# Kernel tuning notes

Measured on AMD Instinct MI355X. Metric: run time of the kernel, lower is better.

Reference implementation:

```python
import jax, jax.numpy as jnp
import numpy as np
from jax import lax

EPS = 1e-10

def _ln(x, g, b):
    m = x.mean(-1, keepdims=True)
    v = x.var(-1, keepdims=True)
    return (x - m) / jnp.sqrt(v + 1e-5) * g + b

def _gather(t, idx):
    # t: (B, HW, c), idx: (B, HW, d) -> (B, HW, d, c); out[n,i,k,:] = t[n, idx[n,i,k], :]
    return jax.vmap(lambda tn, In: tn[In])(t, idx)

def setup_inputs() -> dict:
    key = jax.random.key(0)
    ks = jax.random.split(key, 20)
    b, v, c, d, h, w, hid, ksz = 2, 2, 128, 64, 64, 64, 256, 5
    hw = h * w
    Bf = b * v  # v_1 == 1 target view per reference view
    std = 0.02
    return {
        'features_mv': jax.random.normal(ks[0], (b, v, c, h, w), jnp.float32),
        'warp_indices': jax.random.randint(ks[1], (Bf, hw, d), 0, hw, jnp.int32),
        'depth_prob': jax.random.uniform(ks[2], (Bf, hw, d), jnp.float32),
        'ln1_g': jnp.ones((c,), jnp.float32), 'ln1_b': jnp.zeros((c,), jnp.float32),
        'wq': jax.random.normal(ks[3], (c, c), jnp.float32) * std, 'bq': jnp.zeros((c,), jnp.float32),
        'wk': jax.random.normal(ks[4], (c, c), jnp.float32) * std, 'bk': jnp.zeros((c,), jnp.float32),
        'wv': jax.random.normal(ks[5], (c, c), jnp.float32) * std, 'bv': jnp.zeros((c,), jnp.float32),
        'k_pe': jax.random.normal(ks[6], (1, 1, d), jnp.float32) * std,
        'v_pe': jax.random.normal(ks[7], (1, 1, d), jnp.float32) * std,
        'rpe': jax.random.normal(ks[8], (1, 1, d), jnp.float32) * std,
        'proj_w': jax.random.normal(ks[9], (c, c), jnp.float32) * std, 'proj_b': jnp.zeros((c,), jnp.float32),
        'ln2_g': jnp.ones((c,), jnp.float32), 'ln2_b': jnp.zeros((c,), jnp.float32),
        'fc1_w': jax.random.normal(ks[10], (c, hid), jnp.float32) * std, 'fc1_b': jnp.zeros((hid,), jnp.float32),
        'dw_w': jax.random.normal(ks[11], (hid, 1, ksz, ksz), jnp.float32) * std, 'dw_b': jnp.zeros((hid,), jnp.float32),
        'fc2_w': jax.random.normal(ks[12], (hid, c), jnp.float32) * std, 'fc2_b': jnp.zeros((c,), jnp.float32),
    }

def reference(features_mv, warp_indices, depth_prob, ln1_g, ln1_b, wq, bq, wk, bk, wv, bv,
              k_pe, v_pe, rpe, proj_w, proj_b, ln2_g, ln2_b, fc1_w, fc1_b, dw_w, dw_b, fc2_w, fc2_b):
    b, v, c, h, w = features_mv.shape
    hw = h * w
    hid = fc1_w.shape[1]
    scale = c ** (-0.5)  # num_heads = 1 -> head_dim = dim

    # (b v) (h w) c
    x = features_mv.reshape(b * v, c, hw).transpose(0, 2, 1)
    shortcut = x
    xn = _ln(x, ln1_g, ln1_b)
    q = xn @ wq + bq
    k = xn @ wk + bk
    vv = xn @ wv + bv

    # nn pairing: v=2, v_1=1 -> each reference view attends the other view
    Q = (q.reshape(b, v, hw, c) * scale).reshape(b * v, hw, c)
    K = k.reshape(b, v, hw, c)[:, ::-1].reshape(b * v, hw, c)
    V = vv.reshape(b, v, hw, c)[:, ::-1].reshape(b * v, hw, c)

    # SMM_QmK: cost[n,i,k] = sum_c Q[n,i,c] * K[n, idx[n,i,k], c]
    Kg = _gather(K, warp_indices)                       # (B, hw, d, c)
    cost = jnp.einsum('bic,bikc->bik', Q, Kg)
    Q_pe = Q.sum(-1, keepdims=True)                     # (B, hw, 1)
    cost = cost + Q_pe * k_pe + rpe                     # broadcast (1,1,d)

    # (Sim_UNet similarity refinement omitted: UNetModel source unavailable; identity here)
    attn = jax.nn.softmax(cost, axis=-1)
    attn = attn * depth_prob
    attn = (attn + EPS) / (attn.sum(-1, keepdims=True) + EPS)

    # SMM_AmV: out[n,i,c] = sum_k attn[n,i,k] * V[n, idx[n,i,k], c]
    Vg = _gather(V, warp_indices)                       # (B, hw, d, c)
    out = jnp.einsum('bik,bikc->bic', attn, Vg)
    out = out + (attn * v_pe).sum(-1, keepdims=True)

    # projection + residual (v_1 == 1 so B == b*v)
    x = shortcut + (out @ proj_w + proj_b)

    # ConvFFN residual branch
    xn2 = _ln(x, ln2_g, ln2_b)
    y = jax.nn.gelu(xn2 @ fc1_w + fc1_b, approximate=False)
    yi = y.transpose(0, 2, 1).reshape(b * v, hid, h, w)
    yc = lax.conv_general_dilated(yi, dw_w, (1, 1), 'SAME', feature_group_count=hid,
                                  dimension_numbers=('NCHW', 'OIHW', 'NCHW'))
    yc = jax.nn.gelu(yc + dw_b[None, :, None, None], approximate=False)
    y = y + yc.reshape(b * v, hid, hw).transpose(0, 2, 1)
    y = y @ fc2_w + fc2_b
    return x + y
```

## Files before the change

kernel.cpp:

```cpp
#include <hip/hip_runtime.h>
#include <math.h>

#define TOK   16384
#define HW    4096
#define C     128
#define D     64
#define HID   256

constexpr float LN_EPS = 1e-5f;
constexpr float EPS_R  = 1e-10f;
constexpr float QSCALE = 0.08838834764831845f;

typedef __attribute__((ext_vector_type(8))) short  bf16x8;
typedef __attribute__((ext_vector_type(4))) float  f32x4;
#define MFMA16(a, b, c) __builtin_amdgcn_mfma_f32_16x16x32_bf16((a), (b), (c), 0, 0, 0)

__device__ __forceinline__ float bflo(unsigned u) { return __uint_as_float(u << 16); }
__device__ __forceinline__ float bfhi(unsigned u) { return __uint_as_float(u & 0xffff0000u); }
__device__ __forceinline__ float bfu(unsigned short u) { return __uint_as_float((unsigned)u << 16); }
__device__ __forceinline__ unsigned short f2bf(float f) {
  unsigned u = __float_as_uint(f);
  unsigned r = (u + 0x7fffu + ((u >> 16) & 1u)) >> 16;
  return (unsigned short)r;
}
__device__ __forceinline__ float gelu_exact(float x) {
  return 0.5f * x * (1.0f + erff(x * 0.7071067811865476f));
}

__global__ __launch_bounds__(256) void k_prep(const float* __restrict__ wq,
    const float* __restrict__ wk, const float* __restrict__ wv,
    const float* __restrict__ pw, const float* __restrict__ f1w,
    const float* __restrict__ f2w, unsigned short* __restrict__ wt) {
  int id = blockIdx.x * 256 + threadIdx.x;
  if (id < 16384) {
    int n = id >> 7, k = id & 127;
    wt[id] = f2bf(wq[k * 128 + n]);
  } else if (id < 32768) {
    int e = id - 16384; int n = e >> 7, k = e & 127;
    wt[id] = f2bf(wk[k * 128 + n]);
  } else if (id < 49152) {
    int e = id - 32768; int n = e >> 7, k = e & 127;
    wt[id] = f2bf(wv[k * 128 + n]);
  } else if (id < 65536) {
    int e = id - 49152; int n = e >> 7, k = e & 127;
    wt[id] = f2bf(pw[k * 128 + n]);
  } else if (id < 98304) {
    int e = id - 65536; int n = e >> 7, k = e & 127;
    wt[id] = f2bf(f1w[k * 256 + n]);
  } else if (id < 131072) {
    int e = id - 98304; int n = e >> 8, k = e & 255;
    wt[id] = f2bf(f2w[k * 128 + n]);
  }
}

__global__ __launch_bounds__(256) void k_ln1(const float* __restrict__ feat,
    const float* __restrict__ g, const float* __restrict__ b,
    unsigned short* __restrict__ xnb) {
  __shared__ float tile[64][C + 1];
  int t0 = blockIdx.x * 64;
  int n = t0 / HW, i0 = t0 % HW;
  int tid = threadIdx.x;
  const float* fb = feat + (size_t)n * C * HW;
  for (int e = tid; e < 64 * C; e += 256) {
    int ch = e >> 6, ii = e & 63;
    tile[ii][ch] = fb[(size_t)ch * HW + i0 + ii];
  }
  __syncthreads();
  int wave = tid >> 6, lane = tid & 63;
  for (int tkn = wave; tkn < 64; tkn += 4) {
    float a0 = tile[tkn][lane];
    float a1 = tile[tkn][lane + 64];
    float s = a0 + a1;
    for (int off = 32; off; off >>= 1) s += __shfl_xor(s, off, 64);
    float mean = s * (1.0f / 128.0f);
    float d0 = a0 - mean, d1 = a1 - mean;
    float v = d0 * d0 + d1 * d1;
    for (int off = 32; off; off >>= 1) v += __shfl_xor(v, off, 64);
    float rstd = rsqrtf(v * (1.0f / 128.0f) + LN_EPS);
    size_t ro = (size_t)(t0 + tkn) * C;
    xnb[ro + lane]      = f2bf(d0 * rstd * g[lane] + b[lane]);
    xnb[ro + lane + 64] = f2bf(d1 * rstd * g[lane + 64] + b[lane + 64]);
  }
}

__global__ __launch_bounds__(256) void k_qkv(const unsigned short* __restrict__ xnb,
    const unsigned short* __restrict__ wt,
    const float* __restrict__ bq, const float* __restrict__ bk,
    const float* __restrict__ bv, unsigned short* __restrict__ qb,
    unsigned short* __restrict__ ksw, unsigned short* __restrict__ vsw) {
  int w = threadIdx.x >> 6, lane = threadIdx.x & 63;
  int q4 = lane >> 4, m = lane & 15;
  int t0 = blockIdx.x * 64 + w * 16;
  int wsel = blockIdx.y;
  const unsigned short* Wt = wt + wsel * 16384;
  const unsigned short* ap = xnb + (size_t)(t0 + m) * C + q4 * 8;
  bf16x8 a[4];
  #pragma unroll
  for (int ks = 0; ks < 4; ks++) a[ks] = *(const bf16x8*)(ap + ks * 32);
  f32x4 acc[8];
  #pragma unroll
  for (int nt = 0; nt < 8; nt++) acc[nt] = (f32x4){0.f, 0.f, 0.f, 0.f};
  #pragma unroll
  for (int nt = 0; nt < 8; nt++) {
    const unsigned short* bp = Wt + (size_t)(nt * 16 + m) * C + q4 * 8;
    #pragma unroll
    for (int ks = 0; ks < 4; ks++) {
      bf16x8 bfrag = *(const bf16x8*)(bp + ks * 32);
      acc[nt] = MFMA16(a[ks], bfrag, acc[nt]);
    }
  }
  const float* B = (wsel == 0) ? bq : ((wsel == 1) ? bk : bv);
  float sc = (wsel == 0) ? QSCALE : 1.0f;
  unsigned short* O = (wsel == 0) ? qb : ((wsel == 1) ? ksw : vsw);
  int n = t0 >> 12, i0 = t0 & 4095;
  int base = (wsel == 0) ? t0 : (((n ^ 1) << 12) + i0);
  #pragma unroll
  for (int nt = 0; nt < 8; nt++) {
    int col = nt * 16 + m;
    float bb = B[col];
    #pragma unroll
    for (int reg = 0; reg < 4; reg++) {
      int row = base + q4 * 4 + reg;
      O[(size_t)row * C + col] = f2bf((acc[nt][reg] + bb) * sc);
    }
  }
}

__global__ __launch_bounds__(256) void k_attn(const unsigned short* __restrict__ qb,
    const unsigned short* __restrict__ ksw, const unsigned short* __restrict__ vsw,
    const int* __restrict__ widx, const float* __restrict__ dprob,
    const float* __restrict__ kpe, const float* __restrict__ vpe,
    const float* __restrict__ rpe, unsigned short* __restrict__ aoutb) {
  int lane = threadIdx.x & 63;
  int wave = threadIdx.x >> 6;
  int bid = blockIdx.x;
  int n = (bid >> 1) & 3;
  int within = ((bid >> 3) << 1) | (bid & 1);
  int token = n * HW + within * 4 + wave;
  const unsigned short* Kb = ksw + (size_t)n * HW * C;
  const unsigned short* Vb = vsw + (size_t)n * HW * C;
  int g = lane >> 3, s = lane & 7;
  int myidx = widx[token * D + lane];
  float mydp = dprob[token * D + lane];
  float qreg[16];
  {
    const unsigned short* qp = qb + (size_t)token * C + s * 16;
    uint4 qa = *(const uint4*)(qp);
    uint4 qbv = *(const uint4*)(qp + 8);
    qreg[0] = bflo(qa.x);  qreg[1] = bfhi(qa.x);
    qreg[2] = bflo(qa.y);  qreg[3] = bfhi(qa.y);
    qreg[4] = bflo(qa.z);  qreg[5] = bfhi(qa.z);
    qreg[6] = bflo(qa.w);  qreg[7] = bfhi(qa.w);
    qreg[8] = bflo(qbv.x); qreg[9] = bfhi(qbv.x);
    qreg[10] = bflo(qbv.y); qreg[11] = bfhi(qbv.y);
    qreg[12] = bflo(qbv.z); qreg[13] = bfhi(qbv.z);
    qreg[14] = bflo(qbv.w); qreg[15] = bfhi(qbv.w);
  }
  float qpe = 0.f;
  #pragma unroll
  for (int i = 0; i < 16; i++) qpe += qreg[i];
  qpe += __shfl_xor(qpe, 1, 64);
  qpe += __shfl_xor(qpe, 2, 64);
  qpe += __shfl_xor(qpe, 4, 64);
  int rowv[8];
  #pragma unroll
  for (int pass = 0; pass < 8; ++pass)
    rowv[pass] = __shfl(myidx, pass * 8 + g, 64);
  uint4 ka[8], kb[8];
  #pragma unroll
  for (int pass = 0; pass < 8; ++pass) {
    const unsigned short* kr = Kb + (size_t)rowv[pass] * C + s * 16;
    ka[pass] = *(const uint4*)(kr);
    kb[pass] = *(const uint4*)(kr + 8);
  }
  float mycost = 0.f;
  #pragma unroll
  for (int pass = 0; pass < 8; ++pass) {
    float p;
    p  = bflo(ka[pass].x) * qreg[0]  + bfhi(ka[pass].x) * qreg[1];
    p += bflo(ka[pass].y) * qreg[2]  + bfhi(ka[pass].y) * qreg[3];
    p += bflo(ka[pass].z) * qreg[4]  + bfhi(ka[pass].z) * qreg[5];
    p += bflo(ka[pass].w) * qreg[6]  + bfhi(ka[pass].w) * qreg[7];
    p += bflo(kb[pass].x) * qreg[8]  + bfhi(kb[pass].x) * qreg[9];
    p += bflo(kb[pass].y) * qreg[10] + bfhi(kb[pass].y) * qreg[11];
    p += bflo(kb[pass].z) * qreg[12] + bfhi(kb[pass].z) * qreg[13];
    p += bflo(kb[pass].w) * qreg[14] + bfhi(kb[pass].w) * qreg[15];
    p += __shfl_xor(p, 1, 64);
    p += __shfl_xor(p, 2, 64);
    p += __shfl_xor(p, 4, 64);
    float t = __shfl(p, (lane & 7) << 3, 64);
    if (pass == g) mycost = t;
  }
  mycost += qpe * kpe[lane] + rpe[lane];
  float mx = mycost;
  for (int off = 32; off; off >>= 1) mx = fmaxf(mx, __shfl_xor(mx, off, 64));
  float e = __expf(mycost - mx);
  float ssum = e;
  for (int off = 32; off; off >>= 1) ssum += __shfl_xor(ssum, off, 64);
  float attn = (e / ssum) * mydp;
  float s2 = attn;
  for (int off = 32; off; off >>= 1) s2 += __shfl_xor(s2, off, 64);
  attn = (attn + EPS_R) / (s2 + EPS_R);
  float vpt = attn * vpe[lane];
  for (int off = 32; off; off >>= 1) vpt += __shfl_xor(vpt, off, 64);
  float o0 = vpt, o1 = vpt;
  unsigned att_u = __float_as_uint(attn);
  #pragma unroll
  for (int blk = 0; blk < 8; ++blk) {
    unsigned vv[8];
    #pragma unroll
    for (int j = 0; j < 8; j++) {
      int row = __builtin_amdgcn_readlane(myidx, blk * 8 + j);
      vv[j] = *(const unsigned*)(Vb + (size_t)row * C + lane * 2);
    }
    #pragma unroll
    for (int j = 0; j < 8; j++) {
      float a = __uint_as_float(__builtin_amdgcn_readlane(att_u, blk * 8 + j));
      o0 += a * bflo(vv[j]);
      o1 += a * bfhi(vv[j]);
    }
  }
  unsigned pk = (unsigned)f2bf(o0) | ((unsigned)f2bf(o1) << 16);
  *(unsigned*)(aoutb + (size_t)token * C + lane * 2) = pk;
}

__global__ __launch_bounds__(256) void k_projln(const unsigned short* __restrict__ aoutb,
    const unsigned short* __restrict__ wt, const float* __restrict__ pb,
    const float* __restrict__ feat, float* __restrict__ xio,
    const float* __restrict__ g2, const float* __restrict__ b2,
    unsigned short* __restrict__ xn2b) {
  int w = threadIdx.x >> 6, lane = threadIdx.x & 63;
  int q4 = lane >> 4, m = lane & 15;
  int t0 = blockIdx.x * 64 + w * 16;
  const unsigned short* Wt = wt + 3 * 16384;
  const unsigned short* ap = aoutb + (size_t)(t0 + m) * C + q4 * 8;
  bf16x8 a[4];
  #pragma unroll
  for (int ks = 0; ks < 4; ks++) a[ks] = *(const bf16x8*)(ap + ks * 32);
  f32x4 acc[8];
  #pragma unroll
  for (int nt = 0; nt < 8; nt++) acc[nt] = (f32x4){0.f, 0.f, 0.f, 0.f};
  #pragma unroll
  for (int nt = 0; nt < 8; nt++) {
    const unsigned short* bp = Wt + (size_t)(nt * 16 + m) * C + q4 * 8;
    #pragma unroll
    for (int ks = 0; ks < 4; ks++) {
      bf16x8 bfrag = *(const bf16x8*)(bp + ks * 32);
      acc[nt] = MFMA16(a[ks], bfrag, acc[nt]);
    }
  }
  int nview = t0 >> 12, ibase = (t0 & 4095) + q4 * 4;
  float s1[4] = {0.f, 0.f, 0.f, 0.f}, s2[4] = {0.f, 0.f, 0.f, 0.f};
  #pragma unroll
  for (int nt = 0; nt < 8; nt++) {
    int col = nt * 16 + m;
    float bb = pb[col];
    const float* fp = feat + ((size_t)nview * C + col) * HW + ibase;
    #pragma unroll
    for (int reg = 0; reg < 4; reg++) {
      float v = acc[nt][reg] + bb + fp[reg];
      acc[nt][reg] = v;
      s1[reg] += v;
      s2[reg] += v * v;
    }
  }
  #pragma unroll
  for (int reg = 0; reg < 4; reg++) {
    #pragma unroll
    for (int off = 1; off < 16; off <<= 1) {
      s1[reg] += __shfl_xor(s1[reg], off, 64);
      s2[reg] += __shfl_xor(s2[reg], off, 64);
    }
  }
  float mean[4], rstd[4];
  #pragma unroll
  for (int reg = 0; reg < 4; reg++) {
    mean[reg] = s1[reg] * (1.0f / 128.0f);
    float var = s2[reg] * (1.0f / 128.0f) - mean[reg] * mean[reg];
    rstd[reg] = rsqrtf(var + LN_EPS);
  }
  #pragma unroll
  for (int nt = 0; nt < 8; nt++) {
    int col = nt * 16 + m;
    float gc = g2[col], bc = b2[col];
    #pragma unroll
    for (int reg = 0; reg < 4; reg++) {
      int row = t0 + q4 * 4 + reg;
      float v = acc[nt][reg];
      xio[(size_t)row * C + col] = v;
      xn2b[(size_t)row * C + col] = f2bf((v - mean[reg]) * rstd[reg] * gc + bc);
    }
  }
}

__global__ __launch_bounds__(256) void k_fc1(const unsigned short* __restrict__ xn2b,
    const unsigned short* __restrict__ wt, const float* __restrict__ f1b,
    unsigned short* __restrict__ y) {
  int w = threadIdx.x >> 6, lane = threadIdx.x & 63;
  int q4 = lane >> 4, m = lane & 15;
  int t0 = blockIdx.x * 64 + w * 16;
  int n0 = blockIdx.y * 128;
  const unsigned short* Wt = wt + 65536 + (size_t)n0 * C;
  const unsigned short* ap = xn2b + (size_t)(t0 + m) * C + q4 * 8;
  bf16x8 a[4];
  #pragma unroll
  for (int ks = 0; ks < 4; ks++) a[ks] = *(const bf16x8*)(ap + ks * 32);
  f32x4 acc[8];
  #pragma unroll
  for (int nt = 0; nt < 8; nt++) acc[nt] = (f32x4){0.f, 0.f, 0.f, 0.f};
  #pragma unroll
  for (int nt = 0; nt < 8; nt++) {
    const unsigned short* bp = Wt + (size_t)(nt * 16 + m) * C + q4 * 8;
    #pragma unroll
    for (int ks = 0; ks < 4; ks++) {
      bf16x8 bfrag = *(const bf16x8*)(bp + ks * 32);
      acc[nt] = MFMA16(a[ks], bfrag, acc[nt]);
    }
  }
  #pragma unroll
  for (int nt = 0; nt < 8; nt++) {
    int col = n0 + nt * 16 + m;
    float bb = f1b[col];
    #pragma unroll
    for (int reg = 0; reg < 4; reg++) {
      int row = t0 + q4 * 4 + reg;
      y[(size_t)row * HID + col] = f2bf(gelu_exact(acc[nt][reg] + bb));
    }
  }
}

__global__ __launch_bounds__(256) void k_dwconv(const unsigned short* __restrict__ y,
    const float* __restrict__ w, const float* __restrict__ bias,
    unsigned short* __restrict__ yc) {
  __shared__ float tile[8][401];
  __shared__ float wl[8][25];
  __shared__ float bl[8];
  int bid = blockIdx.x;
  int tile_id = bid & 15;
  int cb = (bid >> 4) & 31;
  int n = bid >> 9;
  int ty = (tile_id >> 2) * 16, tx = (tile_id & 3) * 16;
  int ch0 = cb * 8;
  int tid = threadIdx.x;
  if (tid < 200) wl[tid / 25][tid % 25] = w[(size_t)(ch0 + tid / 25) * 25 + tid % 25];
  if (tid < 8) bl[tid] = bias[ch0 + tid];
  const unsigned short* yb = y + (size_t)n * HW * HID;
  for (int e = tid; e < 400 * 8; e += 256) {
    int cc = e & 7;
    int p = e >> 3;
    int py = p / 20, px = p % 20;
    int gy = ty + py - 2, gx = tx + px - 2;
    float v = 0.f;
    if (gy >= 0 && gy < 64 && gx >= 0 && gx < 64)
      v = bfu(yb[(size_t)(gy * 64 + gx) * HID + ch0 + cc]);
    tile[cc][p] = v;
  }
  __syncthreads();
  int cc = tid & 7;
  int xx = (tid >> 3) & 15;
  int yg = tid >> 7;
  float wreg[25];
  #pragma unroll
  for (int k = 0; k < 25; k++) wreg[k] = wl[cc][k];
  float bb = bl[cc];
  float win[12][5];
  #pragma unroll
  for (int r = 0; r < 12; r++)
    #pragma unroll
    for (int dx = 0; dx < 5; dx++)
      win[r][dx] = tile[cc][(yg * 8 + r) * 20 + xx + dx];
  #pragma unroll
  for (int j = 0; j < 8; ++j) {
    float acc = 0.f;
    #pragma unroll
    for (int dy = 0; dy < 5; ++dy)
      #pragma unroll
      for (int dx = 0; dx < 5; ++dx)
        acc += wreg[dy * 5 + dx] * win[j + dy][dx];
    acc = gelu_exact(acc + bb);
    int yy = yg * 8 + j;
    yc[(size_t)(n * HW + (ty + yy) * 64 + tx + xx) * HID + ch0 + cc] = f2bf(acc);
  }
}

__global__ __launch_bounds__(256) void k_fc2(const unsigned short* __restrict__ y,
    const unsigned short* __restrict__ ycg, const unsigned short* __restrict__ wt,
    const float* __restrict__ f2b, const float* __restrict__ xio,
    float* __restrict__ outp) {
  int w = threadIdx.x >> 6, lane = threadIdx.x & 63;
  int q4 = lane >> 4, m = lane & 15;
  int t0 = blockIdx.x * 64 + w * 16;
  int half = blockIdx.y;
  const unsigned short* Wt = wt + 98304;
  const unsigned short* ap = y + (size_t)(t0 + m) * HID + q4 * 8;
  const unsigned short* cp = ycg + (size_t)(t0 + m) * HID + q4 * 8;
  union U { bf16x8 v; unsigned short s[8]; };
  bf16x8 a[8];
  #pragma unroll
  for (int ks = 0; ks < 8; ks++) {
    U ua, uc, ur;
    ua.v = *(const bf16x8*)(ap + ks * 32);
    uc.v = *(const bf16x8*)(cp + ks * 32);
    #pragma unroll
    for (int j = 0; j < 8; j++) ur.s[j] = f2bf(bfu(ua.s[j]) + bfu(uc.s[j]));
    a[ks] = ur.v;
  }
  f32x4 acc[4];
  #pragma unroll
  for (int nt = 0; nt < 4; nt++) acc[nt] = (f32x4){0.f, 0.f, 0.f, 0.f};
  #pragma unroll
  for (int nt = 0; nt < 4; nt++) {
    const unsigned short* bp = Wt + (size_t)(half * 64 + nt * 16 + m) * HID + q4 * 8;
    #pragma unroll
    for (int ks = 0; ks < 8; ks++) {
      bf16x8 bfrag = *(const bf16x8*)(bp + ks * 32);
      acc[nt] = MFMA16(a[ks], bfrag, acc[nt]);
    }
  }
  #pragma unroll
  for (int nt = 0; nt < 4; nt++) {
    int col = half * 64 + nt * 16 + m;
    float bb = f2b[col];
    #pragma unroll
    for (int reg = 0; reg < 4; reg++) {
      int row = t0 + q4 * 4 + reg;
      outp[(size_t)row * C + col] = acc[nt][reg] + bb + xio[(size_t)row * C + col];
    }
  }
}

extern "C" void kernel_launch(void* const* d_in, const int* in_sizes, int n_in,
                              void* d_out, int out_size, void* d_ws, size_t ws_size,
                              hipStream_t stream) {
  (void)in_sizes; (void)n_in; (void)out_size; (void)ws_size;
  const float* feat  = (const float*)d_in[0];
  const int*   widx  = (const int*)d_in[1];
  const float* dprob = (const float*)d_in[2];
  const float* ln1g  = (const float*)d_in[3];
  const float* ln1b  = (const float*)d_in[4];
  const float* wq    = (const float*)d_in[5];
  const float* bq    = (const float*)d_in[6];
  const float* wk    = (const float*)d_in[7];
  const float* bk    = (const float*)d_in[8];
  const float* wv    = (const float*)d_in[9];
  const float* bv    = (const float*)d_in[10];
  const float* kpe   = (const float*)d_in[11];
  const float* vpe   = (const float*)d_in[12];
  const float* rpe   = (const float*)d_in[13];
  const float* pw    = (const float*)d_in[14];
  const float* pb    = (const float*)d_in[15];
  const float* ln2g  = (const float*)d_in[16];
  const float* ln2b  = (const float*)d_in[17];
  const float* f1w   = (const float*)d_in[18];
  const float* f1b   = (const float*)d_in[19];
  const float* dww   = (const float*)d_in[20];
  const float* dwb   = (const float*)d_in[21];
  const float* f2w   = (const float*)d_in[22];
  const float* f2b   = (const float*)d_in[23];

  float* ws = (float*)d_ws;
  const size_t M2 = (size_t)TOK * C;
  float* xio = ws;
  unsigned short* qbb   = (unsigned short*)(ws + M2);
  unsigned short* xnb   = (unsigned short*)(ws + M2 + M2 / 2);
  unsigned short* ksb   = (unsigned short*)(ws + 2 * M2);
  unsigned short* vsb   = (unsigned short*)(ws + 2 * M2 + M2 / 2);
  unsigned short* aoutb = (unsigned short*)(ws + 3 * M2);
  unsigned short* xn2b  = (unsigned short*)(ws + 3 * M2 + M2 / 2);
  unsigned short* yb    = (unsigned short*)(ws + 4 * M2);
  unsigned short* ycgb  = (unsigned short*)(ws + 5 * M2);
  unsigned short* wtb   = (unsigned short*)(ws + 6 * M2);

  k_prep  <<<512, 256, 0, stream>>>(wq, wk, wv, pw, f1w, f2w, wtb);
  k_ln1   <<<TOK / 64, 256, 0, stream>>>(feat, ln1g, ln1b, xnb);
  k_qkv   <<<dim3(TOK / 64, 3), 256, 0, stream>>>(xnb, wtb, bq, bk, bv, qbb, ksb, vsb);
  k_attn  <<<TOK / 4, 256, 0, stream>>>(qbb, ksb, vsb, widx, dprob, kpe, vpe, rpe, aoutb);
  k_projln<<<TOK / 64, 256, 0, stream>>>(aoutb, wtb, pb, feat, xio, ln2g, ln2b, xn2b);
  k_fc1   <<<dim3(TOK / 64, 2), 256, 0, stream>>>(xn2b, wtb, f1b, yb);
  k_dwconv<<<2048, 256, 0, stream>>>(yb, dww, dwb, ycgb);
  k_fc2   <<<dim3(TOK / 64, 2), 256, 0, stream>>>(yb, ycgb, wtb, f2b, xio, (float*)d_out);
}
```

Baseline: 216.5 us.

## Use fp16 dot2 for Q·K, fuse residual into dwconv, vectorize tile loads

Q and K are now stored as fp16 so the attention dot products can use packed fdot2 instructions in place of unpacking bf16 into scalar FMAs. The depthwise conv kernel now loads 8 channels per pixel with one 16-byte load and writes y + gelu(conv) directly, so fc2 reads one activation tensor instead of two and no longer does the elementwise add. fp16 can overflow where bf16 would not, and the scaled Q and K must stay within fp16 range.

```diff
diff --git a/kernel.cpp b/kernel.cpp
--- a/kernel.cpp
+++ b/kernel.cpp
@@ -13,6 +13,7 @@
 
 typedef __attribute__((ext_vector_type(8))) short  bf16x8;
 typedef __attribute__((ext_vector_type(4))) float  f32x4;
+typedef __attribute__((ext_vector_type(2))) _Float16 half2v;
 #define MFMA16(a, b, c) __builtin_amdgcn_mfma_f32_16x16x32_bf16((a), (b), (c), 0, 0, 0)
 
 __device__ __forceinline__ float bflo(unsigned u) { return __uint_as_float(u << 16); }
@@ -23,9 +24,27 @@
   unsigned r = (u + 0x7fffu + ((u >> 16) & 1u)) >> 16;
   return (unsigned short)r;
 }
+__device__ __forceinline__ unsigned short f2h(float f) {
+  _Float16 h = (_Float16)f;
+  unsigned short r;
+  __builtin_memcpy(&r, &h, 2);
+  return r;
+}
 __device__ __forceinline__ float gelu_exact(float x) {
   return 0.5f * x * (1.0f + erff(x * 0.7071067811865476f));
 }
+
+union U4H { uint4 v; half2v h[4]; };
+
+#if __has_builtin(__builtin_amdgcn_fdot2)
+__device__ __forceinline__ float dot2h(half2v a, half2v b, float c) {
+  return __builtin_amdgcn_fdot2(a, b, c, false);
+}
+#else
+__device__ __forceinline__ float dot2h(half2v a, half2v b, float c) {
+  return c + (float)a.x * (float)b.x + (float)a.y * (float)b.y;
+}
+#endif
 
 __global__ __launch_bounds__(256) void k_prep(const float* __restrict__ wq,
     const float* __restrict__ wk, const float* __restrict__ wv,
@@ -86,7 +105,7 @@
 __global__ __launch_bounds__(256) void k_qkv(const unsigned short* __restrict__ xnb,
     const unsigned short* __restrict__ wt,
     const float* __restrict__ bq, const float* __restrict__ bk,
-    const float* __restrict__ bv, unsigned short* __restrict__ qb,
+    const float* __restrict__ bv, unsigned short* __restrict__ qh,
     unsigned short* __restrict__ ksw, unsigned short* __restrict__ vsw) {
   int w = threadIdx.x >> 6, lane = threadIdx.x & 63;
   int q4 = lane >> 4, m = lane & 15;
@@ -111,7 +130,7 @@
   }
   const float* B = (wsel == 0) ? bq : ((wsel == 1) ? bk : bv);
   float sc = (wsel == 0) ? QSCALE : 1.0f;
-  unsigned short* O = (wsel == 0) ? qb : ((wsel == 1) ? ksw : vsw);
+  unsigned short* O = (wsel == 0) ? qh : ((wsel == 1) ? ksw : vsw);
   int n = t0 >> 12, i0 = t0 & 4095;
   int base = (wsel == 0) ? t0 : (((n ^ 1) << 12) + i0);
   #pragma unroll
@@ -121,12 +140,13 @@
     #pragma unroll
     for (int reg = 0; reg < 4; reg++) {
       int row = base + q4 * 4 + reg;
-      O[(size_t)row * C + col] = f2bf((acc[nt][reg] + bb) * sc);
-    }
-  }
-}
-
-__global__ __launch_bounds__(256) void k_attn(const unsigned short* __restrict__ qb,
+      float v = (acc[nt][reg] + bb) * sc;
+      O[(size_t)row * C + col] = (wsel == 2) ? f2bf(v) : f2h(v);
+    }
+  }
+}
+
+__global__ __launch_bounds__(256) void k_attn(const unsigned short* __restrict__ qh,
     const unsigned short* __restrict__ ksw, const unsigned short* __restrict__ vsw,
     const int* __restrict__ widx, const float* __restrict__ dprob,
     const float* __restrict__ kpe, const float* __restrict__ vpe,
@@ -142,23 +162,19 @@
   int g = lane >> 3, s = lane & 7;
   int myidx = widx[token * D + lane];
   float mydp = dprob[token * D + lane];
-  float qreg[16];
+  half2v qreg[8];
   {
-    const unsigned short* qp = qb + (size_t)token * C + s * 16;
-    uint4 qa = *(const uint4*)(qp);
-    uint4 qbv = *(const uint4*)(qp + 8);
-    qreg[0] = bflo(qa.x);  qreg[1] = bfhi(qa.x);
-    qreg[2] = bflo(qa.y);  qreg[3] = bfhi(qa.y);
-    qreg[4] = bflo(qa.z);  qreg[5] = bfhi(qa.z);
-    qreg[6] = bflo(qa.w);  qreg[7] = bfhi(qa.w);
-    qreg[8] = bflo(qbv.x); qreg[9] = bfhi(qbv.x);
-    qreg[10] = bflo(qbv.y); qreg[11] = bfhi(qbv.y);
-    qreg[12] = bflo(qbv.z); qreg[13] = bfhi(qbv.z);
-    qreg[14] = bflo(qbv.w); qreg[15] = bfhi(qbv.w);
-  }
+    const unsigned short* qp = qh + (size_t)token * C + s * 16;
+    U4H qa, qb2;
+    qa.v = *(const uint4*)(qp);
+    qb2.v = *(const uint4*)(qp + 8);
+    #pragma unroll
+    for (int i = 0; i < 4; i++) { qreg[i] = qa.h[i]; qreg[4 + i] = qb2.h[i]; }
+  }
+  half2v ones = {(_Float16)1.0f, (_Float16)1.0f};
   float qpe = 0.f;
   #pragma unroll
-  for (int i = 0; i < 16; i++) qpe += qreg[i];
+  for (int i = 0; i < 8; i++) qpe = dot2h(qreg[i], ones, qpe);
   qpe += __shfl_xor(qpe, 1, 64);
   qpe += __shfl_xor(qpe, 2, 64);
   qpe += __shfl_xor(qpe, 4, 64);
@@ -176,15 +192,13 @@
   float mycost = 0.f;
   #pragma unroll
   for (int pass = 0; pass < 8; ++pass) {
-    float p;
-    p  = bflo(ka[pass].x) * qreg[0]  + bfhi(ka[pass].x) * qreg[1];
-    p += bflo(ka[pass].y) * qreg[2]  + bfhi(ka[pass].y) * qreg[3];
-    p += bflo(ka[pass].z) * qreg[4]  + bfhi(ka[pass].z) * qreg[5];
-    p += bflo(ka[pass].w) * qreg[6]  + bfhi(ka[pass].w) * qreg[7];
-    p += bflo(kb[pass].x) * qreg[8]  + bfhi(kb[pass].x) * qreg[9];
-    p += bflo(kb[pass].y) * qreg[10] + bfhi(kb[pass].y) * qreg[11];
-    p += bflo(kb[pass].z) * qreg[12] + bfhi(kb[pass].z) * qreg[13];
-    p += bflo(kb[pass].w) * qreg[14] + bfhi(kb[pass].w) * qreg[15];
+    U4H ua, ub;
+    ua.v = ka[pass]; ub.v = kb[pass];
+    float p = 0.f;
+    #pragma unroll
+    for (int i = 0; i < 4; i++) p = dot2h(ua.h[i], qreg[i], p);
+    #pragma unroll
+    for (int i = 0; i < 4; i++) p = dot2h(ub.h[i], qreg[4 + i], p);
     p += __shfl_xor(p, 1, 64);
     p += __shfl_xor(p, 2, 64);
     p += __shfl_xor(p, 4, 64);
@@ -331,7 +345,7 @@
 
 __global__ __launch_bounds__(256) void k_dwconv(const unsigned short* __restrict__ y,
     const float* __restrict__ w, const float* __restrict__ bias,
-    unsigned short* __restrict__ yc) {
+    unsigned short* __restrict__ ysum) {
   __shared__ float tile[8][401];
   __shared__ float wl[8][25];
   __shared__ float bl[8];
@@ -345,15 +359,16 @@
   if (tid < 200) wl[tid / 25][tid % 25] = w[(size_t)(ch0 + tid / 25) * 25 + tid % 25];
   if (tid < 8) bl[tid] = bias[ch0 + tid];
   const unsigned short* yb = y + (size_t)n * HW * HID;
-  for (int e = tid; e < 400 * 8; e += 256) {
-    int cc = e & 7;
-    int p = e >> 3;
+  for (int p = tid; p < 400; p += 256) {
     int py = p / 20, px = p % 20;
     int gy = ty + py - 2, gx = tx + px - 2;
-    float v = 0.f;
+    uint4 v = make_uint4(0u, 0u, 0u, 0u);
     if (gy >= 0 && gy < 64 && gx >= 0 && gx < 64)
-      v = bfu(yb[(size_t)(gy * 64 + gx) * HID + ch0 + cc]);
-    tile[cc][p] = v;
+      v = *(const uint4*)(yb + (size_t)(gy * 64 + gx) * HID + ch0);
+    tile[0][p] = bflo(v.x); tile[1][p] = bfhi(v.x);
+    tile[2][p] = bflo(v.y); tile[3][p] = bfhi(v.y);
+    tile[4][p] = bflo(v.z); tile[5][p] = bfhi(v.z);
+    tile[6][p] = bflo(v.w); tile[7][p] = bfhi(v.w);
   }
   __syncthreads();
   int cc = tid & 7;
@@ -377,34 +392,24 @@
       #pragma unroll
       for (int dx = 0; dx < 5; ++dx)
         acc += wreg[dy * 5 + dx] * win[j + dy][dx];
-    acc = gelu_exact(acc + bb);
+    float o = win[j + 2][2] + gelu_exact(acc + bb);
     int yy = yg * 8 + j;
-    yc[(size_t)(n * HW + (ty + yy) * 64 + tx + xx) * HID + ch0 + cc] = f2bf(acc);
-  }
-}
-
-__global__ __launch_bounds__(256) void k_fc2(const unsigned short* __restrict__ y,
-    const unsigned short* __restrict__ ycg, const unsigned short* __restrict__ wt,
-    const float* __restrict__ f2b, const float* __restrict__ xio,
-    float* __restrict__ outp) {
+    ysum[(size_t)(n * HW + (ty + yy) * 64 + tx + xx) * HID + ch0 + cc] = f2bf(o);
+  }
+}
+
+__global__ __launch_bounds__(256) void k_fc2(const unsigned short* __restrict__ ysum,
+    const unsigned short* __restrict__ wt, const float* __restrict__ f2b,
+    const float* __restrict__ xio, float* __restrict__ outp) {
   int w = threadIdx.x >> 6, lane = threadIdx.x & 63;
   int q4 = lane >> 4, m = lane & 15;
   int t0 = blockIdx.x * 64 + w * 16;
   int half = blockIdx.y;
   const unsigned short* Wt = wt + 98304;
-  const unsigned short* ap = y + (size_t)(t0 + m) * HID + q4 * 8;
-  const unsigned short* cp = ycg + (size_t)(t0 + m) * HID + q4 * 8;
-  union U { bf16x8 v; unsigned short s[8]; };
+  const unsigned short* ap = ysum + (size_t)(t0 + m) * HID + q4 * 8;
   bf16x8 a[8];
   #pragma unroll
-  for (int ks = 0; ks < 8; ks++) {
-    U ua, uc, ur;
-    ua.v = *(const bf16x8*)(ap + ks * 32);
-    uc.v = *(const bf16x8*)(cp + ks * 32);
-    #pragma unroll
-    for (int j = 0; j < 8; j++) ur.s[j] = f2bf(bfu(ua.s[j]) + bfu(uc.s[j]));
-    a[ks] = ur.v;
-  }
+  for (int ks = 0; ks < 8; ks++) a[ks] = *(const bf16x8*)(ap + ks * 32);
   f32x4 acc[4];
   #pragma unroll
   for (int nt = 0; nt < 4; nt++) acc[nt] = (f32x4){0.f, 0.f, 0.f, 0.f};
@@ -461,22 +466,22 @@
   float* ws = (float*)d_ws;
   const size_t M2 = (size_t)TOK * C;
   float* xio = ws;
-  unsigned short* qbb   = (unsigned short*)(ws + M2);
+  unsigned short* qhb   = (unsigned short*)(ws + M2);
   unsigned short* xnb   = (unsigned short*)(ws + M2 + M2 / 2);
   unsigned short* ksb   = (unsigned short*)(ws + 2 * M2);
   unsigned short* vsb   = (unsigned short*)(ws + 2 * M2 + M2 / 2);
   unsigned short* aoutb = (unsigned short*)(ws + 3 * M2);
   unsigned short* xn2b  = (unsigned short*)(ws + 3 * M2 + M2 / 2);
   unsigned short* yb    = (unsigned short*)(ws + 4 * M2);
-  unsigned short* ycgb  = (unsigned short*)(ws + 5 * M2);
+  unsigned short* ysumb = (unsigned short*)(ws + 5 * M2);
   unsigned short* wtb   = (unsigned short*)(ws + 6 * M2);
 
   k_prep  <<<512, 256, 0, stream>>>(wq, wk, wv, pw, f1w, f2w, wtb);
   k_ln1   <<<TOK / 64, 256, 0, stream>>>(feat, ln1g, ln1b, xnb);
-  k_qkv   <<<dim3(TOK / 64, 3), 256, 0, stream>>>(xnb, wtb, bq, bk, bv, qbb, ksb, vsb);
-  k_attn  <<<TOK / 4, 256, 0, stream>>>(qbb, ksb, vsb, widx, dprob, kpe, vpe, rpe, aoutb);
+  k_qkv   <<<dim3(TOK / 64, 3), 256, 0, stream>>>(xnb, wtb, bq, bk, bv, qhb, ksb, vsb);
+  k_attn  <<<TOK / 4, 256, 0, stream>>>(qhb, ksb, vsb, widx, dprob, kpe, vpe, rpe, aoutb);
   k_projln<<<TOK / 64, 256, 0, stream>>>(aoutb, wtb, pb, feat, xio, ln2g, ln2b, xn2b);
   k_fc1   <<<dim3(TOK / 64, 2), 256, 0, stream>>>(xn2b, wtb, f1b, yb);
-  k_dwconv<<<2048, 256, 0, stream>>>(yb, dww, dwb, ycgb);
-  k_fc2   <<<dim3(TOK / 64, 2), 256, 0, stream>>>(yb, ycgb, wtb, f2b, xio, (float*)d_out);
-}
+  k_dwconv<<<2048, 256, 0, stream>>>(yb, dww, dwb, ysumb);
+  k_fc2   <<<dim3(TOK / 64, 2), 256, 0, stream>>>(ysumb, wtb, f2b, xio, (float*)d_out);
+}
```

Result: faster. 211.0 us (-2.6%).
